# Performance work log

Hardware: AMD Instinct MI355X
Metric: run time of the kernel (lower is better)

The kernel has to match this reference:

```python
import jax, jax.numpy as jnp
import numpy as np

LEAK = 0.3
SPECTRAL_RADIUS = 0.9
SPARSITY = 0.9
B, T, IN, H, R, OUT = 64, 512, 256, 512, 512, 10


def _linear_params(key, fan_in, fan_out):
    kw, kb = jax.random.split(key)
    s = 1.0 / np.sqrt(fan_in)
    W = jax.random.uniform(kw, (fan_in, fan_out), jnp.float32, -s, s)
    b = jax.random.uniform(kb, (fan_out,), jnp.float32, -s, s)
    return W, b


def _reservoir(seed, size):
    rng = np.random.default_rng(seed)
    W = rng.standard_normal((size, size)).astype(np.float32)
    mask = rng.random((size, size)) > SPARSITY
    W = W * mask
    rad = np.abs(np.linalg.eigvals(W)).max().real
    return jnp.asarray(W * (SPECTRAL_RADIUS / rad), dtype=jnp.float32)


def setup_inputs() -> dict:
    key = jax.random.key(0)
    keys = jax.random.split(key, 32)
    inp = {}
    inp['x'] = jax.random.normal(keys[0], (B, T, IN), dtype=jnp.float32)
    ki = 1
    for li, lin in [(0, IN), (1, H)]:
        p = f'L{li}_'
        inp[p + 'Win'] = 1.0 * jax.random.normal(keys[ki], (lin, R), dtype=jnp.float32); ki += 1
        inp[p + 'Wres'] = _reservoir(100 + li, R)
        inp[p + 'Wz'], inp[p + 'bz'] = _linear_params(keys[ki], lin + H, H); ki += 1
        inp[p + 'Wr'], inp[p + 'br'] = _linear_params(keys[ki], lin + H, H); ki += 1
        inp[p + 'Wc'], inp[p + 'bc'] = _linear_params(keys[ki], lin + H, H); ki += 1
        inp[p + 'Wg'], inp[p + 'bg'] = _linear_params(keys[ki], lin + H + R, H); ki += 1
        inp[p + 'Wp'], inp[p + 'bp'] = _linear_params(keys[ki], R, H); ki += 1
    inp['Wo1'], inp['bo1'] = _linear_params(keys[ki], H, H); ki += 1
    inp['Wo2'], inp['bo2'] = _linear_params(keys[ki], H, OUT); ki += 1
    return inp


def _run_layer(x, Win, Wres, Wz, bz, Wr, br, Wc, bc, Wg, bg, Wp, bp):
    # x: (B, T, lin) -> outputs (B, T, H)
    b = x.shape[0]
    h0 = jnp.zeros((b, H), x.dtype)
    r0 = jnp.zeros((b, R), x.dtype)

    def step(carry, x_t):
        r, h = carry
        r = (1.0 - LEAK) * r + LEAK * jnp.tanh(x_t @ Win + r @ Wres)
        comb = jnp.concatenate([x_t, h], axis=1)
        z = jax.nn.sigmoid(comb @ Wz + bz)
        reset = jax.nn.sigmoid(comb @ Wr + br)
        cand = jnp.tanh(jnp.concatenate([x_t, reset * h], axis=1) @ Wc + bc)
        h_gru = (1.0 - z) * h + z * cand
        g = jax.nn.sigmoid(jnp.concatenate([x_t, h_gru, r], axis=1) @ Wg + bg)
        h_new = (1.0 - g) * h_gru + g * jnp.tanh(r @ Wp + bp)
        return (r, h_new), h_new

    _, ys = jax.lax.scan(step, (r0, h0), jnp.swapaxes(x, 0, 1))
    return jnp.swapaxes(ys, 0, 1)  # (B, T, H)


def reference(x,
              L0_Win, L0_Wres, L0_Wz, L0_bz, L0_Wr, L0_br, L0_Wc, L0_bc, L0_Wg, L0_bg, L0_Wp, L0_bp,
              L1_Win, L1_Wres, L1_Wz, L1_bz, L1_Wr, L1_br, L1_Wc, L1_bc, L1_Wg, L1_bg, L1_Wp, L1_bp,
              Wo1, bo1, Wo2, bo2):
    h = _run_layer(x, L0_Win, L0_Wres, L0_Wz, L0_bz, L0_Wr, L0_br, L0_Wc, L0_bc, L0_Wg, L0_bg, L0_Wp, L0_bp)
    # dropout p=0.0 (eval) -> identity
    h = _run_layer(h, L1_Win, L1_Wres, L1_Wz, L1_bz, L1_Wr, L1_br, L1_Wc, L1_bc, L1_Wg, L1_bg, L1_Wp, L1_bp)
    last = h[:, -1, :]
    out = jax.nn.relu(last @ Wo1 + bo1) @ Wo2 + bo2
    return out
```

## Files before the change

### kernel.cpp

```cpp
#include <hip/hip_runtime.h>
#include <math.h>

static constexpr int Bsz = 64;
static constexpr int Tt  = 512;
static constexpr int INF = 256;
static constexpr int Hf  = 512;
static constexpr int OUTF = 10;
static constexpr int NBLK = 256;
static constexpr int NTHR = 1024;

__device__ __forceinline__ float sigmoidf_(float x) {
    return 1.0f / (1.0f + __expf(-x));
}

__device__ __forceinline__ float ldc(const float* p) {
    return __hip_atomic_load(const_cast<float*>(p), __ATOMIC_RELAXED, __HIP_MEMORY_SCOPE_AGENT);
}
__device__ __forceinline__ void stc(float* p, float v) {
    __hip_atomic_store(p, v, __ATOMIC_RELAXED, __HIP_MEMORY_SCOPE_AGENT);
}

__device__ __forceinline__ void gsync(unsigned* flags, int myflag, int pollbase, unsigned gen) {
    __syncthreads();
    const int tid = threadIdx.x;
    if (tid == 0)
        __hip_atomic_store(&flags[myflag], gen, __ATOMIC_RELAXED, __HIP_MEMORY_SCOPE_AGENT);
    if (tid < 128) {
        const unsigned* f = &flags[pollbase + tid];
        while (__hip_atomic_load(const_cast<unsigned*>(f), __ATOMIC_RELAXED, __HIP_MEMORY_SCOPE_AGENT) < gen)
            __builtin_amdgcn_s_sleep(2);
    }
    __syncthreads();
}

__global__ __launch_bounds__(256) void transpose_x_k(const float* __restrict__ x,
                                                     float* __restrict__ xT) {
    __shared__ float tile[64][65];
    int t  = blockIdx.x;
    int k0 = blockIdx.y * 64;
    int tid = threadIdx.x;
#pragma unroll
    for (int i = 0; i < 16; ++i) {
        int idx = i * 256 + tid;
        int bb = idx >> 6, kk = idx & 63;
        tile[bb][kk] = x[(size_t)bb * Tt * INF + (size_t)t * INF + k0 + kk];
    }
    __syncthreads();
#pragma unroll
    for (int i = 0; i < 16; ++i) {
        int idx = i * 256 + tid;
        int kk = idx >> 6, bb = idx & 63;
        xT[(size_t)t * INF * 64 + (size_t)(k0 + kk) * 64 + bb] = tile[bb][kk];
    }
}

#define FMA2(a, w, v) { a.x = fmaf((w).x, (v), a.x); a.y = fmaf((w).y, (v), a.y); }

template<int LIN, bool WRITE_Y>
__global__ __launch_bounds__(NTHR, 4) void esn_persist_k(
    const float* __restrict__ xT, float* __restrict__ y,
    float* rA, float* rB, float* hA, float* hB,
    float* rhB, float* hgB,
    const float* __restrict__ Win, const float* __restrict__ Wres,
    const float* __restrict__ Wz, const float* __restrict__ bz,
    const float* __restrict__ Wr, const float* __restrict__ br,
    const float* __restrict__ Wc, const float* __restrict__ bc,
    const float* __restrict__ Wg, const float* __restrict__ bg,
    const float* __restrict__ Wp, const float* __restrict__ bp,
    unsigned* flags)
{
    constexpr int R4 = LIN + 512;
    constexpr int ROWS = 4 * R4 + LIN + 3 * 512;
    constexpr int CX = LIN / 16;

    extern __shared__ char smem[];
    float4* sW  = (float4*)smem;
    float*  pb  = (float*)(smem + (size_t)ROWS * 16);
    float*  lz  = pb + 8192;
    float*  lgx = lz + 128;
    float*  lp  = lgx + 128;
    float*  lgg = lp + 128;
    float*  lhg = lgg + 128;

    const int tid  = threadIdx.x;
    const int lane = tid & 63;
    const int wv   = tid >> 6;
    const int b    = lane & 31;
    const int cs   = lane >> 5;
    const int cg   = blockIdx.x & 127;
    const int bh   = blockIdx.x >> 7;
    const int c0   = cg * 4;
    const int boff = bh * 32;
    const int myflag = bh * 128 + cg;
    const int pollbase = bh * 128;

    float4* wRES = sW;
    float4* wZ   = wRES + R4;
    float4* wR   = wZ + R4;
    float4* wC   = wR + R4;
    float4* wGx  = wC + R4;
    float4* wGh  = wGx + LIN;
    float4* wGr  = wGh + 512;
    float4* wP   = wGr + 512;

    for (int k = tid; k < LIN; k += NTHR) {
        wRES[k] = *(const float4*)&Win[(size_t)k * 512 + c0];
        wGx[k]  = *(const float4*)&Wg[(size_t)k * 512 + c0];
    }
    for (int k = tid; k < R4; k += NTHR) {
        wZ[k] = *(const float4*)&Wz[(size_t)k * 512 + c0];
        wR[k] = *(const float4*)&Wr[(size_t)k * 512 + c0];
        wC[k] = *(const float4*)&Wc[(size_t)k * 512 + c0];
    }
    for (int k = tid; k < 512; k += NTHR) {
        wRES[LIN + k] = *(const float4*)&Wres[(size_t)k * 512 + c0];
        wGh[k] = *(const float4*)&Wg[(size_t)(LIN + k) * 512 + c0];
        wGr[k] = *(const float4*)&Wg[(size_t)(LIN + 512 + k) * 512 + c0];
        wP[k]  = *(const float4*)&Wp[(size_t)k * 512 + c0];
    }
    __syncthreads();

#define W2(base, idx) (((const float2*)(base))[(size_t)(idx) * 2 + cs])

    float* rc = rA; float* rn = rB; float* hc = hA; float* hn = hB;
    unsigned gen = 0;

    for (int t = 0; t < Tt; ++t) {
        const float* xt = xT + (size_t)t * LIN * 64;

        {
            float2 aRES = {0, 0}, aZ = {0, 0}, aR = {0, 0}, aG = {0, 0};
            {
                const float* xb = xt + boff + b;
                int k0 = wv * CX;
#pragma unroll 8
                for (int k = k0; k < k0 + CX; ++k) {
                    float xv = xb[k * 64];
                    float2 w;
                    w = W2(wRES, k); FMA2(aRES, w, xv);
                    w = W2(wZ, k);   FMA2(aZ, w, xv);
                    w = W2(wR, k);   FMA2(aR, w, xv);
                    w = W2(wGx, k);  FMA2(aG, w, xv);
                }
            }
            {
                int k0 = wv * 32;
#pragma unroll 8
                for (int k = k0; k < k0 + 32; ++k) {
                    float rv = ldc(rc + k * 64 + boff + b);
                    float hv = ldc(hc + k * 64 + boff + b);
                    float2 w;
                    w = W2(wRES, LIN + k); FMA2(aRES, w, rv);
                    w = W2(wZ, LIN + k);   FMA2(aZ, w, hv);
                    w = W2(wR, LIN + k);   FMA2(aR, w, hv);
                }
            }
            float2* pb2 = (float2*)pb;
            pb2[(0 * 16 + wv) * 64 + lane] = aRES;
            pb2[(1 * 16 + wv) * 64 + lane] = aZ;
            pb2[(2 * 16 + wv) * 64 + lane] = aR;
            pb2[(3 * 16 + wv) * 64 + lane] = aG;
            __syncthreads();
            if (tid < 512) {
                int m = tid >> 7, rem = tid & 127, c = rem >> 5, bb = rem & 31;
                int pl = (bb + 32 * (c >> 1)) * 2 + (c & 1);
                float s = 0.f;
#pragma unroll
                for (int w = 0; w < 16; ++w) s += pb[(m * 16 + w) * 128 + pl];
                int cab = c0 + c;
                int gi = cab * 64 + boff + bb;
                if (m == 0) {
                    float ro = ldc(rc + gi);
                    stc(rn + gi, 0.7f * ro + 0.3f * tanhf(s));
                } else if (m == 1) {
                    lz[c * 32 + bb] = sigmoidf_(s + bz[cab]);
                } else if (m == 2) {
                    float hv = ldc(hc + gi);
                    stc(rhB + gi, sigmoidf_(s + br[cab]) * hv);
                } else {
                    lgx[c * 32 + bb] = s;
                }
            }
            gsync(flags, myflag, pollbase, ++gen);
        }

        {
            float2 aC = {0, 0}, aP = {0, 0}, aGr = {0, 0};
            {
                const float* xb = xt + boff + b;
                int k0 = wv * CX;
#pragma unroll 8
                for (int k = k0; k < k0 + CX; ++k) {
                    float xv = xb[k * 64];
                    float2 w = W2(wC, k);
                    FMA2(aC, w, xv);
                }
            }
            {
                int k0 = wv * 32;
#pragma unroll 8
                for (int k = k0; k < k0 + 32; ++k) {
                    float rnv = ldc(rn + k * 64 + boff + b);
                    float rhv = ldc(rhB + k * 64 + boff + b);
                    float2 w;
                    w = W2(wC, LIN + k); FMA2(aC, w, rhv);
                    w = W2(wP, k);       FMA2(aP, w, rnv);
                    w = W2(wGr, k);      FMA2(aGr, w, rnv);
                }
            }
            float2* pb2 = (float2*)pb;
            pb2[(0 * 16 + wv) * 64 + lane] = aC;
            pb2[(1 * 16 + wv) * 64 + lane] = aP;
            pb2[(2 * 16 + wv) * 64 + lane] = aGr;
            __syncthreads();
            if (tid < 384) {
                int m = tid >> 7, rem = tid & 127, c = rem >> 5, bb = rem & 31;
                int pl = (bb + 32 * (c >> 1)) * 2 + (c & 1);
                float s = 0.f;
#pragma unroll
                for (int w = 0; w < 16; ++w) s += pb[(m * 16 + w) * 128 + pl];
                int cab = c0 + c;
                int gi = cab * 64 + boff + bb;
                if (m == 0) {
                    float cand = tanhf(s + bc[cab]);
                    float z = lz[c * 32 + bb];
                    float hv = ldc(hc + gi);
                    float hg = (1.f - z) * hv + z * cand;
                    stc(hgB + gi, hg);
                    lhg[c * 32 + bb] = hg;
                } else if (m == 1) {
                    lp[c * 32 + bb] = tanhf(s + bp[cab]);
                } else {
                    lgg[c * 32 + bb] = s + lgx[c * 32 + bb];
                }
            }
            gsync(flags, myflag, pollbase, ++gen);
        }

        {
            float2 aGh = {0, 0};
            {
                int k0 = wv * 32;
#pragma unroll 8
                for (int k = k0; k < k0 + 32; ++k) {
                    float hgv = ldc(hgB + k * 64 + boff + b);
                    float2 w = W2(wGh, k);
                    FMA2(aGh, w, hgv);
                }
            }
            ((float2*)pb)[(0 * 16 + wv) * 64 + lane] = aGh;
            __syncthreads();
            if (tid < 128) {
                int c = tid >> 5, bb = tid & 31;
                int pl = (bb + 32 * (c >> 1)) * 2 + (c & 1);
                float s = 0.f;
#pragma unroll
                for (int w = 0; w < 16; ++w) s += pb[w * 128 + pl];
                int cab = c0 + c;
                int gi = cab * 64 + boff + bb;
                float g = sigmoidf_(s + lgg[c * 32 + bb] + bg[cab]);
                float hgv = lhg[c * 32 + bb];
                float hnv = (1.f - g) * hgv + g * lp[c * 32 + bb];
                stc(hn + gi, hnv);
                if (WRITE_Y) y[(size_t)t * (Hf * 64) + gi] = hnv;
            }
            gsync(flags, myflag, pollbase, ++gen);
        }

        float* tp = rc; rc = rn; rn = tp;
        tp = hc; hc = hn; hn = tp;
    }
#undef W2
}

__global__ __launch_bounds__(256) void head1_k(const float* __restrict__ hlast,
                                               const float* __restrict__ Wo1,
                                               const float* __restrict__ bo1,
                                               float* __restrict__ hidT) {
    int tid = threadIdx.x;
    int b = tid & 63, jg = tid >> 6;
    int j0 = blockIdx.x * 16 + jg * 4;
    float acc[4] = {0.f, 0.f, 0.f, 0.f};
    const float* ap = hlast + b;
    const float* wp = Wo1 + j0;
#pragma unroll 4
    for (int k = 0; k < Hf; ++k) {
        float xv = ap[k * 64];
        const float4 w = *reinterpret_cast<const float4*>(wp + k * 512);
        acc[0] = fmaf(w.x, xv, acc[0]);
        acc[1] = fmaf(w.y, xv, acc[1]);
        acc[2] = fmaf(w.z, xv, acc[2]);
        acc[3] = fmaf(w.w, xv, acc[3]);
    }
#pragma unroll
    for (int jj = 0; jj < 4; ++jj) {
        int j = j0 + jj;
        hidT[j * 64 + b] = fmaxf(acc[jj] + bo1[j], 0.f);
    }
}

__global__ __launch_bounds__(640) void head2_k(const float* __restrict__ hidT,
                                               const float* __restrict__ Wo2,
                                               const float* __restrict__ bo2,
                                               float* __restrict__ out) {
    int tid = threadIdx.x;
    if (tid >= Bsz * OUTF) return;
    int b = tid / OUTF, o = tid % OUTF;
    float acc = 0.f;
    for (int k = 0; k < Hf; ++k)
        acc = fmaf(hidT[k * 64 + b], Wo2[k * OUTF + o], acc);
    out[tid] = acc + bo2[o];
}

struct LayerW {
    const float *Win, *Wres, *Wz, *bz, *Wr, *br, *Wc, *bc, *Wg, *bg, *Wp, *bp;
};

extern "C" void kernel_launch(void* const* d_in, const int* in_sizes, int n_in,
                              void* d_out, int out_size, void* d_ws, size_t ws_size,
                              hipStream_t stream) {
    const float* x = (const float*)d_in[0];
    LayerW L[2];
    int idx = 1;
    for (int li = 0; li < 2; ++li) {
        L[li].Win  = (const float*)d_in[idx++];
        L[li].Wres = (const float*)d_in[idx++];
        L[li].Wz   = (const float*)d_in[idx++];
        L[li].bz   = (const float*)d_in[idx++];
        L[li].Wr   = (const float*)d_in[idx++];
        L[li].br   = (const float*)d_in[idx++];
        L[li].Wc   = (const float*)d_in[idx++];
        L[li].bc   = (const float*)d_in[idx++];
        L[li].Wg   = (const float*)d_in[idx++];
        L[li].bg   = (const float*)d_in[idx++];
        L[li].Wp   = (const float*)d_in[idx++];
        L[li].bp   = (const float*)d_in[idx++];
    }
    const float* Wo1 = (const float*)d_in[idx++];
    const float* bo1 = (const float*)d_in[idx++];
    const float* Wo2 = (const float*)d_in[idx++];
    const float* bo2 = (const float*)d_in[idx++];

    char* ws = (char*)d_ws;
    size_t off = 0;
    auto walloc = [&](size_t bytes) -> float* {
        float* p = (float*)(ws + off);
        off += (bytes + 255) & ~(size_t)255;
        return p;
    };
    const size_t STATE = (size_t)Hf * 64 * sizeof(float);
    float* xT0 = walloc((size_t)Tt * INF * 64 * sizeof(float));
    float* y0  = walloc((size_t)Tt * Hf * 64 * sizeof(float));
    float* rA  = walloc(STATE);
    float* rB  = walloc(STATE);
    float* hA  = walloc(STATE);
    float* hB  = walloc(STATE);
    float* rhB = walloc(STATE);
    float* hgB = walloc(STATE);
    float* hidT = walloc(STATE);
    unsigned* flags = (unsigned*)walloc(NBLK * sizeof(unsigned));
    (void)ws_size;

    constexpr unsigned SMEM0 = (4 * (INF + 512) + INF + 3 * 512) * 16 + 32768 + 5 * 128 * 4;
    constexpr unsigned SMEM1 = (4 * (Hf + 512) + Hf + 3 * 512) * 16 + 32768 + 5 * 128 * 4;
    hipFuncSetAttribute((const void*)esn_persist_k<INF, true>,
                        hipFuncAttributeMaxDynamicSharedMemorySize, SMEM0);
    hipFuncSetAttribute((const void*)esn_persist_k<Hf, false>,
                        hipFuncAttributeMaxDynamicSharedMemorySize, SMEM1);

    transpose_x_k<<<dim3(Tt, INF / 64), 256, 0, stream>>>(x, xT0);

    hipMemsetAsync(flags, 0, NBLK * sizeof(unsigned), stream);
    hipMemsetAsync(rA, 0, STATE, stream);
    hipMemsetAsync(hA, 0, STATE, stream);
    esn_persist_k<INF, true><<<NBLK, NTHR, SMEM0, stream>>>(
        xT0, y0, rA, rB, hA, hB, rhB, hgB,
        L[0].Win, L[0].Wres, L[0].Wz, L[0].bz, L[0].Wr, L[0].br,
        L[0].Wc, L[0].bc, L[0].Wg, L[0].bg, L[0].Wp, L[0].bp, flags);

    hipMemsetAsync(flags, 0, NBLK * sizeof(unsigned), stream);
    hipMemsetAsync(rA, 0, STATE, stream);
    hipMemsetAsync(hA, 0, STATE, stream);
    esn_persist_k<Hf, false><<<NBLK, NTHR, SMEM1, stream>>>(
        y0, nullptr, rA, rB, hA, hB, rhB, hgB,
        L[1].Win, L[1].Wres, L[1].Wz, L[1].bz, L[1].Wr, L[1].br,
        L[1].Wc, L[1].bc, L[1].Wg, L[1].bg, L[1].Wp, L[1].bp, flags);

    head1_k<<<dim3(32, 1), 256, 0, stream>>>(hA, Wo1, bo1, hidT);
    head2_k<<<dim3(1, 1), 640, 0, stream>>>(hidT, Wo2, bo2, (float*)d_out);
}
```

Baseline: 31.07 ms.

## Split grid barrier into arrive/wait, overlap input projections, stage state via LDS

Replaces the combined grid sync with separate arrive and wait phases. The input-dependent x@W products for the next phase or timestep are computed between arrive and wait, which hides them behind the barrier latency. Recurrent state vectors are now loaded cooperatively with 64-bit coherent loads and double-buffered through LDS, replacing per-thread scalar atomic loads. It also switches to a fast exp-based tanh, uses raw s_barrier with explicit waitcnt, and shortens the poll sleep. This costs more register pressure and adds fragile hand-rolled barrier and memory-ordering logic.

```diff
diff --git a/kernel.cpp b/kernel.cpp
--- a/kernel.cpp
+++ b/kernel.cpp
@@ -12,6 +12,12 @@
 __device__ __forceinline__ float sigmoidf_(float x) {
     return 1.0f / (1.0f + __expf(-x));
 }
+__device__ __forceinline__ float tanhf_(float x) {
+    float ax = fabsf(x);
+    float e = __expf(-2.0f * ax);
+    float r = (1.0f - e) / (1.0f + e);
+    return copysignf(r, x);
+}
 
 __device__ __forceinline__ float ldc(const float* p) {
     return __hip_atomic_load(const_cast<float*>(p), __ATOMIC_RELAXED, __HIP_MEMORY_SCOPE_AGENT);
@@ -19,18 +25,29 @@
 __device__ __forceinline__ void stc(float* p, float v) {
     __hip_atomic_store(p, v, __ATOMIC_RELAXED, __HIP_MEMORY_SCOPE_AGENT);
 }
-
-__device__ __forceinline__ void gsync(unsigned* flags, int myflag, int pollbase, unsigned gen) {
-    __syncthreads();
-    const int tid = threadIdx.x;
-    if (tid == 0)
+__device__ __forceinline__ unsigned long long ldcu64(const float* p) {
+    return __hip_atomic_load((unsigned long long*)p, __ATOMIC_RELAXED, __HIP_MEMORY_SCOPE_AGENT);
+}
+
+__device__ __forceinline__ void block_sync_lds() {
+    asm volatile("s_waitcnt lgkmcnt(0)" ::: "memory");
+    __builtin_amdgcn_sched_barrier(0);
+    __builtin_amdgcn_s_barrier();
+}
+__device__ __forceinline__ void arrive(unsigned* flags, int myflag, unsigned gen) {
+    asm volatile("s_waitcnt vmcnt(0) lgkmcnt(0)" ::: "memory");
+    __builtin_amdgcn_sched_barrier(0);
+    __builtin_amdgcn_s_barrier();
+    if (threadIdx.x == 0)
         __hip_atomic_store(&flags[myflag], gen, __ATOMIC_RELAXED, __HIP_MEMORY_SCOPE_AGENT);
-    if (tid < 128) {
-        const unsigned* f = &flags[pollbase + tid];
-        while (__hip_atomic_load(const_cast<unsigned*>(f), __ATOMIC_RELAXED, __HIP_MEMORY_SCOPE_AGENT) < gen)
-            __builtin_amdgcn_s_sleep(2);
-    }
-    __syncthreads();
+}
+__device__ __forceinline__ void waitbar(unsigned* flags, int pollbase, unsigned gen) {
+    if (threadIdx.x < 128) {
+        unsigned* f = &flags[pollbase + threadIdx.x];
+        while (__hip_atomic_load(f, __ATOMIC_RELAXED, __HIP_MEMORY_SCOPE_AGENT) < gen)
+            __builtin_amdgcn_s_sleep(1);
+    }
+    __builtin_amdgcn_s_barrier();
 }
 
 __global__ __launch_bounds__(256) void transpose_x_k(const float* __restrict__ x,
@@ -54,10 +71,36 @@
     }
 }
 
-#define FMA2(a, w, v) { a.x = fmaf((w).x, (v), a.x); a.y = fmaf((w).y, (v), a.y); }
+#define FMA2(a, w, v) { (a).x = fmaf((w).x, (v), (a).x); (a).y = fmaf((w).y, (v), (a).y); }
+#define W2(base, idx) (((const float2*)(base))[(size_t)(idx) * 2 + cs])
+
+template<int LIN>
+__device__ __forceinline__ void xpair(const float* __restrict__ xt, int bidx, int wv, int cs,
+                                      const float4* mA, const float4* mB,
+                                      float2& aA, float2& aB) {
+    const float* xb = xt + bidx;
+    const int k0 = wv * (LIN / 16);
+#pragma unroll 8
+    for (int k = k0; k < k0 + LIN / 16; ++k) {
+        float xv = xb[k * 64];
+        float2 w = W2(mA, k); FMA2(aA, w, xv);
+        w = W2(mB, k);        FMA2(aB, w, xv);
+    }
+}
+template<int LIN>
+__device__ __forceinline__ void xone(const float* __restrict__ xt, int bidx, int wv, int cs,
+                                     const float4* mA, float2& aA) {
+    const float* xb = xt + bidx;
+    const int k0 = wv * (LIN / 16);
+#pragma unroll 8
+    for (int k = k0; k < k0 + LIN / 16; ++k) {
+        float xv = xb[k * 64];
+        float2 w = W2(mA, k); FMA2(aA, w, xv);
+    }
+}
 
 template<int LIN, bool WRITE_Y>
-__global__ __launch_bounds__(NTHR, 4) void esn_persist_k(
+__global__ __launch_bounds__(NTHR) void esn_persist_k(
     const float* __restrict__ xT, float* __restrict__ y,
     float* rA, float* rB, float* hA, float* hB,
     float* rhB, float* hgB,
@@ -71,16 +114,23 @@
 {
     constexpr int R4 = LIN + 512;
     constexpr int ROWS = 4 * R4 + LIN + 3 * 512;
-    constexpr int CX = LIN / 16;
 
     extern __shared__ char smem[];
-    float4* sW  = (float4*)smem;
-    float*  pb  = (float*)(smem + (size_t)ROWS * 16);
-    float*  lz  = pb + 8192;
-    float*  lgx = lz + 128;
-    float*  lp  = lgx + 128;
-    float*  lgg = lp + 128;
-    float*  lhg = lgg + 128;
+    float4* wRES = (float4*)smem;
+    float4* wZ   = wRES + R4;
+    float4* wR   = wZ + R4;
+    float4* wC   = wR + R4;
+    float4* wGx  = wC + R4;
+    float4* wGh  = wGx + LIN;
+    float4* wGr  = wGh + 512;
+    float4* wP   = wGr + 512;
+    float*  stg  = (float*)smem + (size_t)ROWS * 4;
+    float*  pb   = stg;
+    float*  lz   = stg + 8192;
+    float*  lgx  = lz + 128;
+    float*  lp   = lgx + 128;
+    float*  lgg  = lp + 128;
+    float*  lhg  = lgg + 128;
 
     const int tid  = threadIdx.x;
     const int lane = tid & 63;
@@ -91,17 +141,21 @@
     const int bh   = blockIdx.x >> 7;
     const int c0   = cg * 4;
     const int boff = bh * 32;
+    const int bidx = boff + b;
     const int myflag = bh * 128 + cg;
     const int pollbase = bh * 128;
 
-    float4* wRES = sW;
-    float4* wZ   = wRES + R4;
-    float4* wR   = wZ + R4;
-    float4* wC   = wR + R4;
-    float4* wGx  = wC + R4;
-    float4* wGh  = wGx + LIN;
-    float4* wGr  = wGh + 512;
-    float4* wP   = wGr + 512;
+    const int srow = (tid >> 4) & 63;
+    const int sbp  = tid & 15;
+    const int srC0 = tid >> 4;
+
+    const int rm   = tid >> 7;
+    const int rrem = tid & 127;
+    const int rc_  = rrem >> 5;
+    const int rb   = rrem & 31;
+    const int pl   = (rb + 32 * (rc_ >> 1)) * 2 + (rc_ & 1);
+    const int cab  = c0 + rc_;
+    const int gi   = cab * 64 + boff + rb;
 
     for (int k = tid; k < LIN; k += NTHR) {
         wRES[k] = *(const float4*)&Win[(size_t)k * 512 + c0];
@@ -120,157 +174,188 @@
     }
     __syncthreads();
 
-#define W2(base, idx) (((const float2*)(base))[(size_t)(idx) * 2 + cs])
-
     float* rc = rA; float* rn = rB; float* hc = hA; float* hn = hB;
     unsigned gen = 0;
 
+    float2 zx = {0,0}, rsx = {0,0}, resx = {0,0}, gxx = {0,0}, cxx = {0,0};
+    xpair<LIN>(xT, bidx, wv, cs, wZ, wR, zx, rsx);
+    xpair<LIN>(xT, bidx, wv, cs, wRES, wGx, resx, gxx);
+
     for (int t = 0; t < Tt; ++t) {
         const float* xt = xT + (size_t)t * LIN * 64;
 
+        waitbar(flags, pollbase, gen);
+        float rcown = 0.f, hown = 0.f;
+        if (tid < 512) {
+            if (rm == 0) rcown = ldc(rc + gi);
+            else if (rm == 2) hown = ldc(hc + gi);
+        }
         {
-            float2 aRES = {0, 0}, aZ = {0, 0}, aR = {0, 0}, aG = {0, 0};
+            unsigned long long v0, v1, n0 = 0, n1 = 0;
             {
-                const float* xb = xt + boff + b;
-                int k0 = wv * CX;
-#pragma unroll 8
-                for (int k = k0; k < k0 + CX; ++k) {
-                    float xv = xb[k * 64];
+                size_t o0 = (size_t)srow * 64 + boff + sbp * 2;
+                v0 = ldcu64(hc + o0); v1 = ldcu64(rc + o0);
+            }
+            for (int c = 0; c < 8; ++c) {
+                if (c < 7) {
+                    size_t on = (size_t)((c + 1) * 64 + srow) * 64 + boff + sbp * 2;
+                    n0 = ldcu64(hc + on); n1 = ldcu64(rc + on);
+                }
+                float* sbuf = stg + (c & 1) * 4096;
+                *(unsigned long long*)&sbuf[(size_t)srow * 32 + sbp * 2] = v0;
+                *(unsigned long long*)&sbuf[(size_t)(64 + srow) * 32 + sbp * 2] = v1;
+                block_sync_lds();
+                const float* sb = stg + (c & 1) * 4096;
+#pragma unroll
+                for (int rr = 0; rr < 4; ++rr) {
+                    int row = wv * 4 + rr;
+                    float hv = sb[row * 32 + b];
+                    float rv = sb[(64 + row) * 32 + b];
+                    int k = LIN + c * 64 + row;
                     float2 w;
-                    w = W2(wRES, k); FMA2(aRES, w, xv);
-                    w = W2(wZ, k);   FMA2(aZ, w, xv);
-                    w = W2(wR, k);   FMA2(aR, w, xv);
-                    w = W2(wGx, k);  FMA2(aG, w, xv);
-                }
-            }
+                    w = W2(wZ, k);   FMA2(zx, w, hv);
+                    w = W2(wR, k);   FMA2(rsx, w, hv);
+                    w = W2(wRES, k); FMA2(resx, w, rv);
+                }
+                v0 = n0; v1 = n1;
+            }
+        }
+        __builtin_amdgcn_s_barrier();
+        {
+            float2* pb2 = (float2*)pb;
+            pb2[(0 * 16 + wv) * 64 + lane] = resx;
+            pb2[(1 * 16 + wv) * 64 + lane] = zx;
+            pb2[(2 * 16 + wv) * 64 + lane] = rsx;
+            pb2[(3 * 16 + wv) * 64 + lane] = gxx;
+        }
+        block_sync_lds();
+        if (tid < 512) {
+            float s = 0.f;
+#pragma unroll
+            for (int w = 0; w < 16; ++w) s += pb[(rm * 16 + w) * 128 + pl];
+            if (rm == 0)      stc(rn + gi, 0.7f * rcown + 0.3f * tanhf_(s));
+            else if (rm == 1) lz[rrem] = sigmoidf_(s + bz[cab]);
+            else if (rm == 2) stc(rhB + gi, sigmoidf_(s + br[cab]) * hown);
+            else              lgx[rrem] = s;
+        }
+        arrive(flags, myflag, ++gen);
+        cxx.x = 0.f; cxx.y = 0.f;
+        xone<LIN>(xt, bidx, wv, cs, wC, cxx);
+        waitbar(flags, pollbase, gen);
+
+        float hownB = 0.f;
+        if (tid < 128) hownB = ldc(hc + gi);
+        float2 pacc = {0,0}, gracc = {0,0};
+        {
+            unsigned long long v0, v1, n0 = 0, n1 = 0;
             {
-                int k0 = wv * 32;
-#pragma unroll 8
-                for (int k = k0; k < k0 + 32; ++k) {
-                    float rv = ldc(rc + k * 64 + boff + b);
-                    float hv = ldc(hc + k * 64 + boff + b);
+                size_t o0 = (size_t)srow * 64 + boff + sbp * 2;
+                v0 = ldcu64(rn + o0); v1 = ldcu64(rhB + o0);
+            }
+            for (int c = 0; c < 8; ++c) {
+                if (c < 7) {
+                    size_t on = (size_t)((c + 1) * 64 + srow) * 64 + boff + sbp * 2;
+                    n0 = ldcu64(rn + on); n1 = ldcu64(rhB + on);
+                }
+                float* sbuf = stg + (c & 1) * 4096;
+                *(unsigned long long*)&sbuf[(size_t)srow * 32 + sbp * 2] = v0;
+                *(unsigned long long*)&sbuf[(size_t)(64 + srow) * 32 + sbp * 2] = v1;
+                block_sync_lds();
+                const float* sb = stg + (c & 1) * 4096;
+#pragma unroll
+                for (int rr = 0; rr < 4; ++rr) {
+                    int row = wv * 4 + rr;
+                    float rnv = sb[row * 32 + b];
+                    float rhv = sb[(64 + row) * 32 + b];
+                    int k = c * 64 + row;
                     float2 w;
-                    w = W2(wRES, LIN + k); FMA2(aRES, w, rv);
-                    w = W2(wZ, LIN + k);   FMA2(aZ, w, hv);
-                    w = W2(wR, LIN + k);   FMA2(aR, w, hv);
-                }
-            }
+                    w = W2(wC, LIN + k); FMA2(cxx, w, rhv);
+                    w = W2(wP, k);       FMA2(pacc, w, rnv);
+                    w = W2(wGr, k);      FMA2(gracc, w, rnv);
+                }
+                v0 = n0; v1 = n1;
+            }
+        }
+        __builtin_amdgcn_s_barrier();
+        {
             float2* pb2 = (float2*)pb;
-            pb2[(0 * 16 + wv) * 64 + lane] = aRES;
-            pb2[(1 * 16 + wv) * 64 + lane] = aZ;
-            pb2[(2 * 16 + wv) * 64 + lane] = aR;
-            pb2[(3 * 16 + wv) * 64 + lane] = aG;
-            __syncthreads();
-            if (tid < 512) {
-                int m = tid >> 7, rem = tid & 127, c = rem >> 5, bb = rem & 31;
-                int pl = (bb + 32 * (c >> 1)) * 2 + (c & 1);
-                float s = 0.f;
-#pragma unroll
-                for (int w = 0; w < 16; ++w) s += pb[(m * 16 + w) * 128 + pl];
-                int cab = c0 + c;
-                int gi = cab * 64 + boff + bb;
-                if (m == 0) {
-                    float ro = ldc(rc + gi);
-                    stc(rn + gi, 0.7f * ro + 0.3f * tanhf(s));
-                } else if (m == 1) {
-                    lz[c * 32 + bb] = sigmoidf_(s + bz[cab]);
-                } else if (m == 2) {
-                    float hv = ldc(hc + gi);
-                    stc(rhB + gi, sigmoidf_(s + br[cab]) * hv);
-                } else {
-                    lgx[c * 32 + bb] = s;
-                }
-            }
-            gsync(flags, myflag, pollbase, ++gen);
-        }
-
+            pb2[(0 * 16 + wv) * 64 + lane] = cxx;
+            pb2[(1 * 16 + wv) * 64 + lane] = pacc;
+            pb2[(2 * 16 + wv) * 64 + lane] = gracc;
+        }
+        block_sync_lds();
+        if (tid < 384) {
+            float s = 0.f;
+#pragma unroll
+            for (int w = 0; w < 16; ++w) s += pb[(rm * 16 + w) * 128 + pl];
+            if (rm == 0) {
+                float cand = tanhf_(s + bc[cab]);
+                float zv = lz[rrem];
+                float hg = (1.f - zv) * hownB + zv * cand;
+                stc(hgB + gi, hg);
+                lhg[rrem] = hg;
+            } else if (rm == 1) {
+                lp[rrem] = tanhf_(s + bp[cab]);
+            } else {
+                lgg[rrem] = s + lgx[rrem];
+            }
+        }
+        arrive(flags, myflag, ++gen);
+        gxx.x = 0.f; gxx.y = 0.f; resx.x = 0.f; resx.y = 0.f;
+        if (t + 1 < Tt)
+            xpair<LIN>(xT + (size_t)(t + 1) * LIN * 64, bidx, wv, cs, wRES, wGx, resx, gxx);
+        waitbar(flags, pollbase, gen);
+
+        float2 ghacc = {0,0};
         {
-            float2 aC = {0, 0}, aP = {0, 0}, aGr = {0, 0};
+            unsigned long long v0, v1, n0 = 0, n1 = 0;
             {
-                const float* xb = xt + boff + b;
-                int k0 = wv * CX;
-#pragma unroll 8
-                for (int k = k0; k < k0 + CX; ++k) {
-                    float xv = xb[k * 64];
-                    float2 w = W2(wC, k);
-                    FMA2(aC, w, xv);
-                }
-            }
-            {
-                int k0 = wv * 32;
-#pragma unroll 8
-                for (int k = k0; k < k0 + 32; ++k) {
-                    float rnv = ldc(rn + k * 64 + boff + b);
-                    float rhv = ldc(rhB + k * 64 + boff + b);
-                    float2 w;
-                    w = W2(wC, LIN + k); FMA2(aC, w, rhv);
-                    w = W2(wP, k);       FMA2(aP, w, rnv);
-                    w = W2(wGr, k);      FMA2(aGr, w, rnv);
-                }
-            }
-            float2* pb2 = (float2*)pb;
-            pb2[(0 * 16 + wv) * 64 + lane] = aC;
-            pb2[(1 * 16 + wv) * 64 + lane] = aP;
-            pb2[(2 * 16 + wv) * 64 + lane] = aGr;
-            __syncthreads();
-            if (tid < 384) {
-                int m = tid >> 7, rem = tid & 127, c = rem >> 5, bb = rem & 31;
-                int pl = (bb + 32 * (c >> 1)) * 2 + (c & 1);
-                float s = 0.f;
-#pragma unroll
-                for (int w = 0; w < 16; ++w) s += pb[(m * 16 + w) * 128 + pl];
-                int cab = c0 + c;
-                int gi = cab * 64 + boff + bb;
-                if (m == 0) {
-                    float cand = tanhf(s + bc[cab]);
-                    float z = lz[c * 32 + bb];
-                    float hv = ldc(hc + gi);
-                    float hg = (1.f - z) * hv + z * cand;
-                    stc(hgB + gi, hg);
-                    lhg[c * 32 + bb] = hg;
-                } else if (m == 1) {
-                    lp[c * 32 + bb] = tanhf(s + bp[cab]);
-                } else {
-                    lgg[c * 32 + bb] = s + lgx[c * 32 + bb];
-                }
-            }
-            gsync(flags, myflag, pollbase, ++gen);
-        }
-
-        {
-            float2 aGh = {0, 0};
-            {
-                int k0 = wv * 32;
-#pragma unroll 8
-                for (int k = k0; k < k0 + 32; ++k) {
-                    float hgv = ldc(hgB + k * 64 + boff + b);
+                size_t o0 = (size_t)srC0 * 64 + boff + sbp * 2;
+                size_t o1 = (size_t)(64 + srC0) * 64 + boff + sbp * 2;
+                v0 = ldcu64(hgB + o0); v1 = ldcu64(hgB + o1);
+            }
+            for (int c = 0; c < 4; ++c) {
+                if (c < 3) {
+                    size_t on0 = (size_t)((c + 1) * 128 + srC0) * 64 + boff + sbp * 2;
+                    size_t on1 = (size_t)((c + 1) * 128 + 64 + srC0) * 64 + boff + sbp * 2;
+                    n0 = ldcu64(hgB + on0); n1 = ldcu64(hgB + on1);
+                }
+                float* sbuf = stg + (c & 1) * 4096;
+                *(unsigned long long*)&sbuf[(size_t)srC0 * 32 + sbp * 2] = v0;
+                *(unsigned long long*)&sbuf[(size_t)(64 + srC0) * 32 + sbp * 2] = v1;
+                block_sync_lds();
+                const float* sb = stg + (c & 1) * 4096;
+#pragma unroll
+                for (int rr = 0; rr < 8; ++rr) {
+                    int row = wv * 8 + rr;
+                    float hgv = sb[row * 32 + b];
+                    int k = c * 128 + row;
                     float2 w = W2(wGh, k);
-                    FMA2(aGh, w, hgv);
-                }
-            }
-            ((float2*)pb)[(0 * 16 + wv) * 64 + lane] = aGh;
-            __syncthreads();
-            if (tid < 128) {
-                int c = tid >> 5, bb = tid & 31;
-                int pl = (bb + 32 * (c >> 1)) * 2 + (c & 1);
-                float s = 0.f;
-#pragma unroll
-                for (int w = 0; w < 16; ++w) s += pb[w * 128 + pl];
-                int cab = c0 + c;
-                int gi = cab * 64 + boff + bb;
-                float g = sigmoidf_(s + lgg[c * 32 + bb] + bg[cab]);
-                float hgv = lhg[c * 32 + bb];
-                float hnv = (1.f - g) * hgv + g * lp[c * 32 + bb];
-                stc(hn + gi, hnv);
-                if (WRITE_Y) y[(size_t)t * (Hf * 64) + gi] = hnv;
-            }
-            gsync(flags, myflag, pollbase, ++gen);
-        }
+                    FMA2(ghacc, w, hgv);
+                }
+                v0 = n0; v1 = n1;
+            }
+        }
+        __builtin_amdgcn_s_barrier();
+        ((float2*)pb)[(0 * 16 + wv) * 64 + lane] = ghacc;
+        block_sync_lds();
+        if (tid < 128) {
+            float s = 0.f;
+#pragma unroll
+            for (int w = 0; w < 16; ++w) s += pb[w * 128 + pl];
+            float g = sigmoidf_(s + lgg[rrem] + bg[cab]);
+            float hnv = (1.f - g) * lhg[rrem] + g * lp[rrem];
+            stc(hn + gi, hnv);
+            if (WRITE_Y) y[(size_t)t * (Hf * 64) + gi] = hnv;
+        }
+        arrive(flags, myflag, ++gen);
+        zx.x = 0.f; zx.y = 0.f; rsx.x = 0.f; rsx.y = 0.f;
+        if (t + 1 < Tt)
+            xpair<LIN>(xT + (size_t)(t + 1) * LIN * 64, bidx, wv, cs, wZ, wR, zx, rsx);
 
         float* tp = rc; rc = rn; rn = tp;
         tp = hc; hc = hn; hn = tp;
     }
-#undef W2
 }
 
 __global__ __launch_bounds__(256) void head1_k(const float* __restrict__ hlast,
@@ -361,8 +446,8 @@
     unsigned* flags = (unsigned*)walloc(NBLK * sizeof(unsigned));
     (void)ws_size;
 
-    constexpr unsigned SMEM0 = (4 * (INF + 512) + INF + 3 * 512) * 16 + 32768 + 5 * 128 * 4;
-    constexpr unsigned SMEM1 = (4 * (Hf + 512) + Hf + 3 * 512) * 16 + 32768 + 5 * 128 * 4;
+    constexpr unsigned SMEM0 = (5 * INF + 3584) * 16 + 32768 + 2560;
+    constexpr unsigned SMEM1 = (5 * Hf  + 3584) * 16 + 32768 + 2560;
     hipFuncSetAttribute((const void*)esn_persist_k<INF, true>,
                         hipFuncAttributeMaxDynamicSharedMemorySize, SMEM0);
     hipFuncSetAttribute((const void*)esn_persist_k<Hf, false>,
```

Result: slower. 50.27 ms (+61.8%).
